# Kernel tuning notes

Hardware: AMD Instinct MI355X
Metric: run time of the kernel (lower is better)

## Reference

```python
import jax, jax.numpy as jnp
import numpy as np

MAX_DISP = 192

def _conv(x, w, b=None, stride=1, pad=0):
    y = jax.lax.conv_general_dilated(x, w, (stride, stride), [(pad, pad), (pad, pad)],
                                     dimension_numbers=('NCHW', 'OIHW', 'NCHW'))
    return y if b is None else y + b[None, :, None, None]

def _inorm(x):  # InstanceNorm2d, affine=False
    m = x.mean((2, 3), keepdims=True)
    v = x.var((2, 3), keepdims=True)
    return (x - m) * jax.lax.rsqrt(v + 1e-5)

def _bnorm(x):  # BatchNorm2d at init (gamma=1, beta=0), batch stats
    m = x.mean((0, 2, 3), keepdims=True)
    v = x.var((0, 2, 3), keepdims=True)
    return (x - m) * jax.lax.rsqrt(v + 1e-5)

def _encoder(x, w1, b1, w2, b2, w3, b3, norm):
    # simplified BasicEncoder: two stride-2 convs -> 1/4 resolution, then 1x1 proj
    x = jax.nn.relu(norm(_conv(x, w1, b1, 2, 3)))
    x = jax.nn.relu(norm(_conv(x, w2, b2, 2, 1)))
    return _conv(x, w3, b3, 1, 0)

def _forward(image1, image2, fnet_w1, fnet_b1, fnet_w2, fnet_b2, fnet_w3, fnet_b3,
             cnet_w1, cnet_b1, cnet_w2, cnet_b2, cnet_w3, cnet_b3,
             bform_a, bform_b, bform_cd_w, bform_cd_b,
             gru_wz, gru_bz, gru_wr, gru_br, gru_wq, gru_bq,
             disp_w1, disp_b1, disp_w2, disp_b2):
    i1 = 2.0 * (image1 / 255.0) - 1.0
    i2 = 2.0 * (image2 / 255.0) - 1.0
    fmap1 = _encoder(i1, fnet_w1, fnet_b1, fnet_w2, fnet_b2, fnet_w3, fnet_b3, _inorm)
    fmap2 = _encoder(i2, fnet_w1, fnet_b1, fnet_w2, fnet_b2, fnet_w3, fnet_b3, _inorm)
    hidden = jnp.tanh(_encoder(i1, cnet_w1, cnet_b1, cnet_w2, cnet_b2, cnet_w3, cnet_b3, _bnorm))
    Wf = fmap1.shape[3]
    for d in range(MAX_DISP // 4):  # 48 sequential width-sweep steps, shrinking overlap
        f1 = fmap1[:, :, :, d:]
        f2 = fmap2[:, :, :, :Wf - d] if d > 0 else fmap2
        # BilinearForm: a(x) + b(y) + cd(x*y), all 1x1 convs
        feat = _conv(f1, bform_a) + _conv(f2, bform_b) + _conv(f1 * f2, bform_cd_w, bform_cd_b)
        h = hidden[:, :, :, d:]
        # gru_input = cat(h, feat); ConvGRU cats hidden again -> [h, h, feat] = 96 ch
        hx = jnp.concatenate([h, h, feat], axis=1)
        z = jax.nn.sigmoid(_conv(hx, gru_wz, gru_bz, 1, 1))
        r = jax.nn.sigmoid(_conv(hx, gru_wr, gru_br, 1, 1))
        q = jnp.tanh(_conv(jnp.concatenate([r * h, h, feat], axis=1), gru_wq, gru_bq, 1, 1))
        h = (1.0 - z) * h + z * q
        hidden = hidden.at[:, :, :, d:].set(h)  # in-place scatter back
    # DisparityHead: conv3x3 -> relu -> conv3x3, negated
    return -_conv(jax.nn.relu(_conv(hidden, disp_w1, disp_b1, 1, 1)), disp_w2, disp_b2, 1, 1)

def setup_inputs():
    key = jax.random.key(0)
    ks = jax.random.split(key, 16)
    B, H, W, D = 1, 384, 640, 32
    def n(k, shape, scale=0.05):
        return (jax.random.normal(k, shape) * scale).astype(jnp.float32)
    z = lambda c: jnp.zeros((c,), jnp.float32)
    return {
        'image1': jax.random.uniform(ks[0], (B, 3, H, W), jnp.float32) * 255.0,
        'image2': jax.random.uniform(ks[1], (B, 3, H, W), jnp.float32) * 255.0,
        'fnet_w1': n(ks[2], (D, 3, 7, 7)), 'fnet_b1': z(D),
        'fnet_w2': n(ks[3], (D, D, 3, 3)), 'fnet_b2': z(D),
        'fnet_w3': n(ks[4], (D, D, 1, 1)), 'fnet_b3': z(D),
        'cnet_w1': n(ks[5], (D, 3, 7, 7)), 'cnet_b1': z(D),
        'cnet_w2': n(ks[6], (D, D, 3, 3)), 'cnet_b2': z(D),
        'cnet_w3': n(ks[7], (D, D, 1, 1)), 'cnet_b3': z(D),
        'bform_a': n(ks[8], (D, D, 1, 1)), 'bform_b': n(ks[9], (D, D, 1, 1)),
        'bform_cd_w': n(ks[10], (D, D, 1, 1)), 'bform_cd_b': z(D),
        'gru_wz': n(ks[11], (D, 3 * D, 3, 3)), 'gru_bz': z(D),
        'gru_wr': n(ks[12], (D, 3 * D, 3, 3)), 'gru_br': z(D),
        'gru_wq': n(ks[13], (D, 3 * D, 3, 3)), 'gru_bq': z(D),
        'disp_w1': n(ks[14], (64, D, 3, 3)), 'disp_b1': z(64),
        'disp_w2': n(ks[15], (1, 64, 3, 3)), 'disp_b2': z(1),
    }

def reference(image1, image2, fnet_w1, fnet_b1, fnet_w2, fnet_b2, fnet_w3, fnet_b3,
              cnet_w1, cnet_b1, cnet_w2, cnet_b2, cnet_w3, cnet_b3,
              bform_a, bform_b, bform_cd_w, bform_cd_b,
              gru_wz, gru_bz, gru_wr, gru_br, gru_wq, gru_bq,
              disp_w1, disp_b1, disp_w2, disp_b2):
    return _forward(image1, image2, fnet_w1, fnet_b1, fnet_w2, fnet_b2, fnet_w3, fnet_b3,
                    cnet_w1, cnet_b1, cnet_w2, cnet_b2, cnet_w3, cnet_b3,
                    bform_a, bform_b, bform_cd_w, bform_cd_b,
                    gru_wz, gru_bz, gru_wr, gru_br, gru_wq, gru_bq,
                    disp_w1, disp_b1, disp_w2, disp_b2)
```

## Files before the change

### kernel.cpp

```cpp
#include <hip/hip_runtime.h>
#include <math.h>

#define H0 384
#define W0 640
#define H1 192
#define W1 320
#define H2 96
#define W2 160
#define NP1 (H1*W1)
#define NP2 (H2*W2)
#define ND  48
#define NBLK2 (NP2/256)
#define CHW ((size_t)32*NP2)
#define PW 162
#define PH 98
#define PSL (PH*PW)
#define PCHW ((size_t)32*PSL)

typedef float v2f __attribute__((ext_vector_type(2)));


__global__ void zero_buf_kernel(float* __restrict__ p, size_t n) {
    size_t i = (size_t)blockIdx.x*256 + threadIdx.x;
    size_t stride = (size_t)gridDim.x*256;
    for (; i < n; i += stride) p[i] = 0.f;
}

__global__ void transpose_w_kernel(const float* __restrict__ in, float* __restrict__ out,
                                   int CI, int K, int CO) {
    int idx = blockIdx.x*256 + threadIdx.x;
    int total = CI*K*CO;
    if (idx >= total) return;
    int co = idx % CO;
    int t  = idx / CO;
    int k  = t % K;
    int ci = t / K;
    out[idx] = in[(co*CI + ci)*K + k];
}

__global__ void prep_zr_pk(const float* __restrict__ wz, const float* __restrict__ wr,
                           float4* __restrict__ wpk) {
    int idx = blockIdx.x*256 + threadIdx.x;
    if (idx >= 16*64*9) return;
    int k  = idx % 9;
    int ci = (idx/9) % 64;
    int cg = idx / (9*64);
    int co0 = cg*2, co1 = co0 + 1;
    float z0, z1, r0, r1;
    if (ci < 32) {
        z0 = wz[(co0*96 + ci)*9 + k] + wz[(co0*96 + ci + 32)*9 + k];
        z1 = wz[(co1*96 + ci)*9 + k] + wz[(co1*96 + ci + 32)*9 + k];
        r0 = wr[(co0*96 + ci)*9 + k] + wr[(co0*96 + ci + 32)*9 + k];
        r1 = wr[(co1*96 + ci)*9 + k] + wr[(co1*96 + ci + 32)*9 + k];
    } else {
        z0 = wz[(co0*96 + ci + 32)*9 + k];
        z1 = wz[(co1*96 + ci + 32)*9 + k];
        r0 = wr[(co0*96 + ci + 32)*9 + k];
        r1 = wr[(co1*96 + ci + 32)*9 + k];
    }
    wpk[idx] = make_float4(z0, z1, r0, r1);
}

__global__ void prep_q_pk(const float* __restrict__ wq, float2* __restrict__ qpk) {
    int idx = blockIdx.x*256 + threadIdx.x;
    if (idx >= 16*96*9) return;
    int k  = idx % 9;
    int ci = (idx/9) % 96;
    int cg = idx / (9*96);
    qpk[idx] = make_float2(wq[((cg*2)*96 + ci)*9 + k], wq[((cg*2+1)*96 + ci)*9 + k]);
}

__global__ void pad_init_kernel(const float* __restrict__ hidden, float* __restrict__ hwork) {
    int idx = blockIdx.x*256 + threadIdx.x;
    if (idx >= 32*PSL) return;
    int c = idx / PSL;
    int r = idx % PSL;
    int py = r / PW, px = r % PW;
    int y = py - 1, x = px - 1;
    float v = 0.f;
    if ((unsigned)y < (unsigned)H2 && (unsigned)x < (unsigned)W2)
        v = hidden[c*NP2 + y*W2 + x];
    hwork[idx] = v;
}


__global__ void conv7s2_v2(const float* __restrict__ img, const float* __restrict__ wt,
                           const float* __restrict__ b, float* __restrict__ out) {
    int sp = blockIdx.x*256 + threadIdx.x;
    int oy = sp / W1, ox = sp % W1;
    float acc[32];
    #pragma unroll
    for (int j = 0; j < 32; ++j) acc[j] = b[j];
    for (int ci = 0; ci < 3; ++ci) {
        for (int ky = 0; ky < 7; ++ky) {
            int iy = 2*oy - 3 + ky;
            if ((unsigned)iy >= (unsigned)H0) continue;
            const float* row  = img + ci*(H0*W0) + iy*W0;
            const float* wrow = wt + (ci*49 + ky*7)*32;
            #pragma unroll
            for (int kx = 0; kx < 7; ++kx) {
                int ix = 2*ox - 3 + kx;
                if ((unsigned)ix >= (unsigned)W0) continue;
                float v = row[ix]*(2.0f/255.0f) - 1.0f;
                const float4* wp = (const float4*)(wrow + kx*32);
                #pragma unroll
                for (int j4 = 0; j4 < 8; ++j4) {
                    float4 w4 = wp[j4];
                    acc[4*j4+0] += v*w4.x; acc[4*j4+1] += v*w4.y;
                    acc[4*j4+2] += v*w4.z; acc[4*j4+3] += v*w4.w;
                }
            }
        }
    }
    #pragma unroll
    for (int j = 0; j < 32; ++j) out[j*NP1 + sp] = acc[j];
}

__global__ void stats_partial_kernel(const float* __restrict__ x, int N, float* __restrict__ st) {
    int c = blockIdx.x >> 3, sl = blockIdx.x & 7;
    int chunk = N >> 3;
    const float4* p = (const float4*)(x + (size_t)c*N + (size_t)sl*chunk);
    int n4 = chunk >> 2;
    float s = 0.f, s2 = 0.f;
    for (int i = threadIdx.x; i < n4; i += 256) {
        float4 v = p[i];
        s  += v.x + v.y + v.z + v.w;
        s2 += v.x*v.x + v.y*v.y + v.z*v.z + v.w*v.w;
    }
    __shared__ float sh1[256], sh2[256];
    sh1[threadIdx.x] = s; sh2[threadIdx.x] = s2;
    __syncthreads();
    for (int o = 128; o > 0; o >>= 1) {
        if (threadIdx.x < o) { sh1[threadIdx.x] += sh1[threadIdx.x+o]; sh2[threadIdx.x] += sh2[threadIdx.x+o]; }
        __syncthreads();
    }
    if (threadIdx.x == 0) { atomicAdd(&st[2*c], sh1[0]); atomicAdd(&st[2*c+1], sh2[0]); }
}

__global__ void norm_relu_v2(float* __restrict__ x, const float* __restrict__ st, int N) {
    int c = blockIdx.y;
    float m    = st[2*c] / (float)N;
    float var  = st[2*c+1] / (float)N - m*m;
    float rstd = rsqrtf(var + 1e-5f);
    float4* p = (float4*)(x + (size_t)c*N);
    int i = blockIdx.x*256 + threadIdx.x;
    float4 v = p[i];
    v.x = fmaxf((v.x-m)*rstd, 0.f); v.y = fmaxf((v.y-m)*rstd, 0.f);
    v.z = fmaxf((v.z-m)*rstd, 0.f); v.w = fmaxf((v.w-m)*rstd, 0.f);
    p[i] = v;
}

__global__ void conv3s2_v2(const float* __restrict__ in, const float* __restrict__ wt,
                           const float* __restrict__ b, float* __restrict__ out) {
    int cg = blockIdx.x / (NP2/256);
    int sp = (blockIdx.x % (NP2/256))*256 + threadIdx.x;
    int co8 = cg*8;
    int oy = sp / W2, ox = sp % W2;
    float acc[8];
    #pragma unroll
    for (int j = 0; j < 8; ++j) acc[j] = b[co8+j];
    for (int ci = 0; ci < 32; ++ci) {
        const float* ip  = in + ci*NP1;
        const float* wci = wt + ci*9*32 + co8;
        #pragma unroll
        for (int ky = 0; ky < 3; ++ky) {
            int iy = 2*oy - 1 + ky;
            if ((unsigned)iy >= (unsigned)H1) continue;
            const float* row = ip + iy*W1;
            #pragma unroll
            for (int kx = 0; kx < 3; ++kx) {
                int ix = 2*ox - 1 + kx;
                if ((unsigned)ix >= (unsigned)W1) continue;
                float v = row[ix];
                const float4* wp = (const float4*)(wci + (ky*3+kx)*32);
                float4 w0 = wp[0], w1 = wp[1];
                acc[0] += v*w0.x; acc[1] += v*w0.y; acc[2] += v*w0.z; acc[3] += v*w0.w;
                acc[4] += v*w1.x; acc[5] += v*w1.y; acc[6] += v*w1.z; acc[7] += v*w1.w;
            }
        }
    }
    #pragma unroll
    for (int j = 0; j < 8; ++j) out[(co8+j)*NP2 + sp] = acc[j];
}

__global__ void conv1x1_v2(const float* __restrict__ in, const float* __restrict__ wt,
                           const float* __restrict__ b, float* __restrict__ out, int mode) {
    int cg = blockIdx.x / (NP2/256);
    int sp = (blockIdx.x % (NP2/256))*256 + threadIdx.x;
    int co8 = cg*8;
    float acc[8];
    #pragma unroll
    for (int j = 0; j < 8; ++j) acc[j] = b[co8+j];
    for (int ci = 0; ci < 32; ++ci) {
        float v = in[ci*NP2 + sp];
        const float4* wp = (const float4*)(wt + ci*32 + co8);
        float4 w0 = wp[0], w1 = wp[1];
        acc[0] += v*w0.x; acc[1] += v*w0.y; acc[2] += v*w0.z; acc[3] += v*w0.w;
        acc[4] += v*w1.x; acc[5] += v*w1.y; acc[6] += v*w1.z; acc[7] += v*w1.w;
    }
    #pragma unroll
    for (int j = 0; j < 8; ++j) {
        float a = acc[j];
        if (mode) a = tanhf(a);
        out[(co8+j)*NP2 + sp] = a;
    }
}


__global__ void feat0_pad_kernel(const float* __restrict__ fmap1, const float* __restrict__ fmap2,
                                 const float* __restrict__ wat, const float* __restrict__ wbt,
                                 const float* __restrict__ wct, const float* __restrict__ bc,
                                 float* __restrict__ featA) {
    int cg  = blockIdx.x / NBLK2;
    int sp  = (blockIdx.x % NBLK2)*256 + threadIdx.x;
    int y = sp / W2;
    int gx = sp % W2;
    int co8 = cg*8;
    float acc[8];
    #pragma unroll
    for (int j = 0; j < 8; ++j) acc[j] = bc[co8+j];
    for (int ci = 0; ci < 32; ++ci) {
        float f1 = fmap1[ci*NP2 + sp];
        float f2 = fmap2[ci*NP2 + sp];
        float f12 = f1*f2;
        const float4* ap = (const float4*)(wat + ci*32 + co8);
        const float4* bp = (const float4*)(wbt + ci*32 + co8);
        const float4* cp = (const float4*)(wct + ci*32 + co8);
        float4 a0 = ap[0], a1 = ap[1];
        float4 b0 = bp[0], b1 = bp[1];
        float4 c0 = cp[0], c1 = cp[1];
        acc[0] += f1*a0.x + f2*b0.x + f12*c0.x;
        acc[1] += f1*a0.y + f2*b0.y + f12*c0.y;
        acc[2] += f1*a0.z + f2*b0.z + f12*c0.z;
        acc[3] += f1*a0.w + f2*b0.w + f12*c0.w;
        acc[4] += f1*a1.x + f2*b1.x + f12*c1.x;
        acc[5] += f1*a1.y + f2*b1.y + f12*c1.y;
        acc[6] += f1*a1.z + f2*b1.z + f12*c1.z;
        acc[7] += f1*a1.w + f2*b1.w + f12*c1.w;
    }
    float* dst = featA + (size_t)(y+1)*PW + (gx+1);
    #pragma unroll
    for (int j = 0; j < 8; ++j) dst[(size_t)(co8+j)*PSL] = acc[j];
}


__global__ __launch_bounds__(256, 4)
void zrf_v5(const float* __restrict__ hworkA, const float* __restrict__ featA,
            const float* __restrict__ fmap1, const float* __restrict__ fmap2,
            const float4* __restrict__ wzrpk,
            const float* __restrict__ wat, const float* __restrict__ wbt,
            const float* __restrict__ wct, const float* __restrict__ bfc,
            const float* __restrict__ bz, const float* __restrict__ br,
            float* __restrict__ zbuf, float* __restrict__ rhpad,
            float* __restrict__ featB, int d) {
    __shared__ v2f lwz[64*9], lwr[64*9];
    __shared__ v2f lfa[32], lfb[32], lfc[32];
    int cg  = blockIdx.x / 30;
    int sp2 = (blockIdx.x % 30)*256 + threadIdx.x;
    int co0 = cg*2;
    {
        const float4* wsrc = wzrpk + (size_t)cg*576;
        for (int i = threadIdx.x; i < 576; i += 256) {
            float4 w = wsrc[i];
            lwz[i] = (v2f){w.x, w.y};
            lwr[i] = (v2f){w.z, w.w};
        }
        if (threadIdx.x < 32) {
            int ci = threadIdx.x;
            lfa[ci] = (v2f){wat[ci*32+co0], wat[ci*32+co0+1]};
            lfb[ci] = (v2f){wbt[ci*32+co0], wbt[ci*32+co0+1]};
            lfc[ci] = (v2f){wct[ci*32+co0], wct[ci*32+co0+1]};
        }
    }
    __syncthreads();
    int y0 = (sp2 / W2)*2;
    int gx = sp2 % W2;
    size_t poff = (size_t)(y0+1)*PW + (gx+1);

    if (gx == d-1) {
        #pragma unroll
        for (int j = 0; j < 2; ++j) {
            rhpad[(size_t)(co0+j)*PSL + poff]      = 0.f;
            rhpad[(size_t)(co0+j)*PSL + poff + PW] = 0.f;
        }
    }

    int dn = d + 1;
    if (dn < ND) {
        if (gx == dn-1) {
            #pragma unroll
            for (int j = 0; j < 2; ++j) {
                featB[(size_t)(co0+j)*PSL + poff]      = 0.f;
                featB[(size_t)(co0+j)*PSL + poff + PW] = 0.f;
            }
        } else if (gx >= dn) {
            v2f f0 = (v2f){bfc[co0], bfc[co0+1]};
            v2f f1 = f0;
            int base1 = y0*W2 + gx;
            #pragma unroll 2
            for (int ci = 0; ci < 32; ++ci) {
                float a1 = fmap1[ci*NP2 + base1];
                float a2 = fmap1[ci*NP2 + base1 + W2];
                float b1 = fmap2[ci*NP2 + base1 - dn];
                float b2 = fmap2[ci*NP2 + base1 + W2 - dn];
                v2f wa = lfa[ci], wb = lfb[ci], wc = lfc[ci];
                f0 += wa*(v2f){a1,a1} + wb*(v2f){b1,b1} + wc*(v2f){a1*b1,a1*b1};
                f1 += wa*(v2f){a2,a2} + wb*(v2f){b2,b2} + wc*(v2f){a2*b2,a2*b2};
            }
            featB[(size_t)co0*PSL + poff]          = f0.x;
            featB[(size_t)(co0+1)*PSL + poff]      = f0.y;
            featB[(size_t)co0*PSL + poff + PW]     = f1.x;
            featB[(size_t)(co0+1)*PSL + poff + PW] = f1.y;
        }
    }

    if (gx < d) return;

    v2f az0 = (v2f){bz[co0], bz[co0+1]}, az1 = az0;
    v2f ar0 = (v2f){br[co0], br[co0+1]}, ar1 = ar0;
    #pragma unroll
    for (int pass = 0; pass < 2; ++pass) {
        const float* p = (pass == 0 ? hworkA : featA) + poff;
        const v2f* wz = lwz + pass*288;
        const v2f* wr = lwr + pass*288;
        #pragma unroll 2
        for (int ci = 0; ci < 32; ++ci) {
            float v[12];
            #pragma unroll
            for (int r = 0; r < 4; ++r) {
                v[r*3+0] = p[(r-1)*PW - 1];
                v[r*3+1] = p[(r-1)*PW    ];
                v[r*3+2] = p[(r-1)*PW + 1];
            }
            #pragma unroll
            for (int k = 0; k < 9; ++k) {
                int ky = k/3, kx = k - 3*ky;
                float t0 = v[ky*3+kx];
                float t1 = v[(ky+1)*3+kx];
                v2f wzk = wz[k], wrk = wr[k];
                az0 += wzk*(v2f){t0,t0}; az1 += wzk*(v2f){t1,t1};
                ar0 += wrk*(v2f){t0,t0}; ar1 += wrk*(v2f){t1,t1};
            }
            p += PSL;
            wz += 9; wr += 9;
        }
    }
    v2f z0, z1, r0, r1;
    z0.x = 1.f/(1.f + __expf(-az0.x)); z0.y = 1.f/(1.f + __expf(-az0.y));
    z1.x = 1.f/(1.f + __expf(-az1.x)); z1.y = 1.f/(1.f + __expf(-az1.y));
    r0.x = 1.f/(1.f + __expf(-ar0.x)); r0.y = 1.f/(1.f + __expf(-ar0.y));
    r1.x = 1.f/(1.f + __expf(-ar1.x)); r1.y = 1.f/(1.f + __expf(-ar1.y));
    int ub = y0*W2 + gx;
    float h00 = hworkA[(size_t)co0*PSL + poff];
    float h01 = hworkA[(size_t)(co0+1)*PSL + poff];
    float h10 = hworkA[(size_t)co0*PSL + poff + PW];
    float h11 = hworkA[(size_t)(co0+1)*PSL + poff + PW];
    zbuf[(size_t)co0*NP2 + ub]          = z0.x;
    zbuf[(size_t)(co0+1)*NP2 + ub]      = z0.y;
    zbuf[(size_t)co0*NP2 + ub + W2]     = z1.x;
    zbuf[(size_t)(co0+1)*NP2 + ub + W2] = z1.y;
    rhpad[(size_t)co0*PSL + poff]          = r0.x*h00;
    rhpad[(size_t)(co0+1)*PSL + poff]      = r0.y*h01;
    rhpad[(size_t)co0*PSL + poff + PW]     = r1.x*h10;
    rhpad[(size_t)(co0+1)*PSL + poff + PW] = r1.y*h11;
}

__global__ __launch_bounds__(256, 4)
void qup_v5(const float* __restrict__ rhpad, const float* __restrict__ hworkA,
            const float* __restrict__ featA, const float* __restrict__ zbuf,
            const float2* __restrict__ qpk, const float* __restrict__ bq,
            float* __restrict__ hidden, float* __restrict__ hworkB, int d) {
    __shared__ v2f lw[96*9];
    int cg  = blockIdx.x / 30;
    int sp2 = (blockIdx.x % 30)*256 + threadIdx.x;
    int co0 = cg*2;
    {
        const float2* wsrc = qpk + (size_t)cg*864;
        for (int i = threadIdx.x; i < 864; i += 256) {
            float2 w = wsrc[i];
            lw[i] = (v2f){w.x, w.y};
        }
    }
    __syncthreads();
    int y0 = (sp2 / W2)*2;
    int gx = sp2 % W2;
    size_t poff = (size_t)(y0+1)*PW + (gx+1);

    if (gx < d) {
        #pragma unroll
        for (int j = 0; j < 2; ++j) {
            size_t p0 = (size_t)(co0+j)*PSL + poff;
            hworkB[p0]      = hworkA[p0];
            hworkB[p0 + PW] = hworkA[p0 + PW];
        }
        return;
    }

    v2f a0 = (v2f){bq[co0], bq[co0+1]};
    v2f a1 = a0;
    const float* bases[3];
    bases[0] = rhpad; bases[1] = hworkA; bases[2] = featA;
    #pragma unroll
    for (int pass = 0; pass < 3; ++pass) {
        const float* p = bases[pass] + poff;
        const v2f* wp = lw + pass*288;
        #pragma unroll 2
        for (int ci = 0; ci < 32; ++ci) {
            float v[12];
            #pragma unroll
            for (int r = 0; r < 4; ++r) {
                v[r*3+0] = p[(r-1)*PW - 1];
                v[r*3+1] = p[(r-1)*PW    ];
                v[r*3+2] = p[(r-1)*PW + 1];
            }
            #pragma unroll
            for (int k = 0; k < 9; ++k) {
                int ky = k/3, kx = k - 3*ky;
                float t0 = v[ky*3+kx];
                float t1 = v[(ky+1)*3+kx];
                v2f wk = wp[k];
                a0 += wk*(v2f){t0,t0};
                a1 += wk*(v2f){t1,t1};
            }
            p += PSL;
            wp += 9;
        }
    }
    float q00 = tanhf(a0.x), q01 = tanhf(a0.y);
    float q10 = tanhf(a1.x), q11 = tanhf(a1.y);
    int ub = y0*W2 + gx;
    #pragma unroll
    for (int j = 0; j < 2; ++j) {
        float qa = (j == 0) ? q00 : q01;
        float qb = (j == 0) ? q10 : q11;
        size_t pidx = (size_t)(co0+j)*PSL + poff;
        size_t uidx = (size_t)(co0+j)*NP2 + ub;
        float z_a = zbuf[uidx];
        float z_b = zbuf[uidx + W2];
        float h_a = hworkA[pidx];
        float h_b = hworkA[pidx + PW];
        float hn_a = (1.f - z_a)*h_a + z_a*qa;
        float hn_b = (1.f - z_b)*h_b + z_b*qb;
        hidden[uidx]      = hn_a;
        hidden[uidx + W2] = hn_b;
        hworkB[pidx]      = (gx == d) ? 0.f : hn_a;
        hworkB[pidx + PW] = (gx == d) ? 0.f : hn_b;
    }
}


__global__ void disp1_v2(const float* __restrict__ hidden, const float* __restrict__ wt,
                         const float* __restrict__ b, float* __restrict__ out) {
    int cg = blockIdx.x / (NP2/256);
    int sp = (blockIdx.x % (NP2/256))*256 + threadIdx.x;
    int co8 = cg*8;
    int y = sp / W2, x = sp % W2;
    float acc[8];
    #pragma unroll
    for (int j = 0; j < 8; ++j) acc[j] = b[co8+j];
    for (int ci = 0; ci < 32; ++ci) {
        const float* ip = hidden + ci*NP2;
        #pragma unroll
        for (int dy = 0; dy < 3; ++dy) {
            int ys = y + dy - 1;
            if ((unsigned)ys >= (unsigned)H2) continue;
            const float* row = ip + ys*W2;
            #pragma unroll
            for (int dx = 0; dx < 3; ++dx) {
                int xs = x + dx - 1;
                if ((unsigned)xs >= (unsigned)W2) continue;
                float v = row[xs];
                const float4* wp = (const float4*)(wt + (ci*9 + dy*3 + dx)*64 + co8);
                float4 w0 = wp[0], w1 = wp[1];
                acc[0] += v*w0.x; acc[1] += v*w0.y; acc[2] += v*w0.z; acc[3] += v*w0.w;
                acc[4] += v*w1.x; acc[5] += v*w1.y; acc[6] += v*w1.z; acc[7] += v*w1.w;
            }
        }
    }
    #pragma unroll
    for (int j = 0; j < 8; ++j) out[(co8+j)*NP2 + sp] = fmaxf(acc[j], 0.f);
}

__global__ void disp2_part_kernel(const float* __restrict__ in, const float* __restrict__ w,
                                  float* __restrict__ part) {
    __shared__ float lw[8*9];
    int g  = blockIdx.x / NBLK2;
    int sp = (blockIdx.x % NBLK2)*256 + threadIdx.x;
    if (threadIdx.x < 72) lw[threadIdx.x] = w[g*72 + threadIdx.x];
    __syncthreads();
    int y = sp / W2, x = sp % W2;
    float acc = 0.f;
    #pragma unroll
    for (int ci = 0; ci < 8; ++ci) {
        const float* ip = in + (g*8 + ci)*NP2;
        #pragma unroll
        for (int dy = 0; dy < 3; ++dy) {
            int ys = y+dy-1; if ((unsigned)ys >= (unsigned)H2) continue;
            const float* row = ip + ys*W2;
            #pragma unroll
            for (int dx = 0; dx < 3; ++dx) {
                int xs = x+dx-1; if ((unsigned)xs >= (unsigned)W2) continue;
                acc += lw[ci*9+dy*3+dx] * row[xs];
            }
        }
    }
    part[g*NP2 + sp] = acc;
}

__global__ void disp2_comb_kernel(const float* __restrict__ part, const float* __restrict__ b,
                                  float* __restrict__ out) {
    int sp = blockIdx.x*256 + threadIdx.x;
    float acc = b[0];
    #pragma unroll
    for (int g = 0; g < 8; ++g) acc += part[g*NP2 + sp];
    out[sp] = -acc;
}


extern "C" void kernel_launch(void* const* d_in, const int* in_sizes, int n_in,
                              void* d_out, int out_size, void* d_ws, size_t ws_size,
                              hipStream_t stream) {
    const float* image1   = (const float*)d_in[0];
    const float* image2   = (const float*)d_in[1];
    const float* fnet_w1  = (const float*)d_in[2];
    const float* fnet_b1  = (const float*)d_in[3];
    const float* fnet_w2  = (const float*)d_in[4];
    const float* fnet_b2  = (const float*)d_in[5];
    const float* fnet_w3  = (const float*)d_in[6];
    const float* fnet_b3  = (const float*)d_in[7];
    const float* cnet_w1  = (const float*)d_in[8];
    const float* cnet_b1  = (const float*)d_in[9];
    const float* cnet_w2  = (const float*)d_in[10];
    const float* cnet_b2  = (const float*)d_in[11];
    const float* cnet_w3  = (const float*)d_in[12];
    const float* cnet_b3  = (const float*)d_in[13];
    const float* bform_a  = (const float*)d_in[14];
    const float* bform_b  = (const float*)d_in[15];
    const float* bform_cd_w = (const float*)d_in[16];
    const float* bform_cd_b = (const float*)d_in[17];
    const float* gru_wz   = (const float*)d_in[18];
    const float* gru_bz   = (const float*)d_in[19];
    const float* gru_wr   = (const float*)d_in[20];
    const float* gru_br   = (const float*)d_in[21];
    const float* gru_wq   = (const float*)d_in[22];
    const float* gru_bq   = (const float*)d_in[23];
    const float* disp_w1  = (const float*)d_in[24];
    const float* disp_b1  = (const float*)d_in[25];
    const float* disp_w2  = (const float*)d_in[26];
    const float* disp_b2  = (const float*)d_in[27];

    float* ws = (float*)d_ws;
    size_t o = 0;
    float* e1     = ws + o; o += (size_t)32*NP1;
    float* e2     = ws + o; o += CHW;
    float* fmap1  = ws + o; o += CHW;
    float* fmap2  = ws + o; o += CHW;
    float* hidden = ws + o; o += CHW;
    float* zbuf   = ws + o; o += CHW;
    float* hwork0 = ws + o; o += PCHW;
    float* hwork1 = ws + o; o += PCHW;
    float* rhpad  = ws + o; o += PCHW;
    float* feat0  = ws + o; o += PCHW;
    float* feat1  = ws + o; o += PCHW;
    float* stats  = ws + o; o += 384;
    float* wzrpk  = ws + o; o += 16*64*9*4;
    float* wqpk   = ws + o; o += 16*96*9*2;
    float* we1f   = ws + o; o += 3*49*32;
    float* we1c   = ws + o; o += 3*49*32;
    float* we2f   = ws + o; o += 32*9*32;
    float* we2c   = ws + o; o += 32*9*32;
    float* w3f    = ws + o; o += 32*32;
    float* w3c    = ws + o; o += 32*32;
    float* wat    = ws + o; o += 32*32;
    float* wbt    = ws + o; o += 32*32;
    float* wct    = ws + o; o += 32*32;
    float* wd1t   = ws + o; o += 32*9*64;
    float* disp1buf  = e1;
    float* disp2part = e2;

    zero_buf_kernel<<<2, 256, 0, stream>>>(stats, 384);
    transpose_w_kernel<<<(3*49*32+255)/256, 256, 0, stream>>>(fnet_w1, we1f, 3, 49, 32);
    transpose_w_kernel<<<(3*49*32+255)/256, 256, 0, stream>>>(cnet_w1, we1c, 3, 49, 32);
    transpose_w_kernel<<<(32*9*32+255)/256, 256, 0, stream>>>(fnet_w2, we2f, 32, 9, 32);
    transpose_w_kernel<<<(32*9*32+255)/256, 256, 0, stream>>>(cnet_w2, we2c, 32, 9, 32);
    transpose_w_kernel<<<4, 256, 0, stream>>>(fnet_w3, w3f, 32, 1, 32);
    transpose_w_kernel<<<4, 256, 0, stream>>>(cnet_w3, w3c, 32, 1, 32);
    transpose_w_kernel<<<4, 256, 0, stream>>>(bform_a, wat, 32, 1, 32);
    transpose_w_kernel<<<4, 256, 0, stream>>>(bform_b, wbt, 32, 1, 32);
    transpose_w_kernel<<<4, 256, 0, stream>>>(bform_cd_w, wct, 32, 1, 32);
    transpose_w_kernel<<<(32*9*64+255)/256, 256, 0, stream>>>(disp_w1, wd1t, 32, 9, 64);
    prep_zr_pk<<<(16*64*9+255)/256, 256, 0, stream>>>(gru_wz, gru_wr, (float4*)wzrpk);
    prep_q_pk<<<(16*96*9+255)/256, 256, 0, stream>>>(gru_wq, (float2*)wqpk);

    auto encoder = [&](const float* img, const float* w1t, const float* b1,
                       const float* w2t, const float* b2,
                       const float* w3t, const float* b3, float* dst, int mode,
                       float* st1, float* st2) {
        conv7s2_v2<<<NP1/256, 256, 0, stream>>>(img, w1t, b1, e1);
        stats_partial_kernel<<<256, 256, 0, stream>>>(e1, NP1, st1);
        norm_relu_v2<<<dim3(NP1/1024, 32), 256, 0, stream>>>(e1, st1, NP1);
        conv3s2_v2<<<4*(NP2/256), 256, 0, stream>>>(e1, w2t, b2, e2);
        stats_partial_kernel<<<256, 256, 0, stream>>>(e2, NP2, st2);
        norm_relu_v2<<<dim3(NP2/1024, 32), 256, 0, stream>>>(e2, st2, NP2);
        conv1x1_v2<<<4*(NP2/256), 256, 0, stream>>>(e2, w3t, b3, dst, mode);
    };
    encoder(image1, we1f, fnet_b1, we2f, fnet_b2, w3f, fnet_b3, fmap1, 0, stats+0,   stats+64);
    encoder(image2, we1f, fnet_b1, we2f, fnet_b2, w3f, fnet_b3, fmap2, 0, stats+128, stats+192);
    encoder(image1, we1c, cnet_b1, we2c, cnet_b2, w3c, cnet_b3, hidden, 1, stats+256, stats+320);

    pad_init_kernel<<<(32*PSL+255)/256, 256, 0, stream>>>(hidden, hwork0);
    zero_buf_kernel<<<1024, 256, 0, stream>>>(hwork1, PCHW);
    zero_buf_kernel<<<1024, 256, 0, stream>>>(rhpad, PCHW);
    zero_buf_kernel<<<1024, 256, 0, stream>>>(feat0, PCHW);
    zero_buf_kernel<<<1024, 256, 0, stream>>>(feat1, PCHW);
    feat0_pad_kernel<<<4*NBLK2, 256, 0, stream>>>(fmap1, fmap2, wat, wbt, wct,
                                                  bform_cd_b, feat0);

    float* hwA = hwork0; float* hwB = hwork1;
    float* ftA = feat0;  float* ftB = feat1;
    for (int d = 0; d < ND; ++d) {
        zrf_v5<<<16*30, 256, 0, stream>>>(hwA, ftA, fmap1, fmap2, (const float4*)wzrpk,
                                          wat, wbt, wct, bform_cd_b, gru_bz, gru_br,
                                          zbuf, rhpad, ftB, d);
        qup_v5<<<16*30, 256, 0, stream>>>(rhpad, hwA, ftA, zbuf, (const float2*)wqpk,
                                          gru_bq, hidden, hwB, d);
        float* t;
        t = hwA; hwA = hwB; hwB = t;
        t = ftA; ftA = ftB; ftB = t;
    }

    disp1_v2<<<8*(NP2/256), 256, 0, stream>>>(hidden, wd1t, disp_b1, disp1buf);
    disp2_part_kernel<<<8*NBLK2, 256, 0, stream>>>(disp1buf, disp_w2, disp2part);
    disp2_comb_kernel<<<NBLK2, 256, 0, stream>>>(disp2part, disp_b2, (float*)d_out);
}
```

Measured before the change: 3.103 ms.

## Shrink GRU sweep grids to active width, fuse prep kernels, retile encoder and disp convs

The 48 GRU sweep steps now launch grids sized to the shrinking active width (W2-d) and index from column d, so blocks no longer idle on columns already finished and qup no longer copies inactive columns. Final hidden state goes into a padded buffer that the new disp1 kernel reads without bounds checks, caching its weights in LDS and computing two rows per thread. The separate weight-prep and zeroing launches are merged into one kernel and one larger zero pass. The first encoder conv is split across two output-channel groups to raise parallelism. The hfinal buffer only receives interior writes on active columns, so correctness depends on its zeroing and on each column's final write landing at the right step.

```diff
diff --git a/kernel.cpp b/kernel.cpp
--- a/kernel.cpp
+++ b/kernel.cpp
@@ -26,11 +26,8 @@
     for (; i < n; i += stride) p[i] = 0.f;
 }
 
-__global__ void transpose_w_kernel(const float* __restrict__ in, float* __restrict__ out,
-                                   int CI, int K, int CO) {
-    int idx = blockIdx.x*256 + threadIdx.x;
-    int total = CI*K*CO;
-    if (idx >= total) return;
+__device__ __forceinline__ void twr_dev(const float* __restrict__ in, float* __restrict__ out,
+                                        int idx, int CI, int K, int CO) {
     int co = idx % CO;
     int t  = idx / CO;
     int k  = t % K;
@@ -38,36 +35,71 @@
     out[idx] = in[(co*CI + ci)*K + k];
 }
 
-__global__ void prep_zr_pk(const float* __restrict__ wz, const float* __restrict__ wr,
-                           float4* __restrict__ wpk) {
-    int idx = blockIdx.x*256 + threadIdx.x;
-    if (idx >= 16*64*9) return;
-    int k  = idx % 9;
-    int ci = (idx/9) % 64;
-    int cg = idx / (9*64);
-    int co0 = cg*2, co1 = co0 + 1;
-    float z0, z1, r0, r1;
-    if (ci < 32) {
-        z0 = wz[(co0*96 + ci)*9 + k] + wz[(co0*96 + ci + 32)*9 + k];
-        z1 = wz[(co1*96 + ci)*9 + k] + wz[(co1*96 + ci + 32)*9 + k];
-        r0 = wr[(co0*96 + ci)*9 + k] + wr[(co0*96 + ci + 32)*9 + k];
-        r1 = wr[(co1*96 + ci)*9 + k] + wr[(co1*96 + ci + 32)*9 + k];
-    } else {
-        z0 = wz[(co0*96 + ci + 32)*9 + k];
-        z1 = wz[(co1*96 + ci + 32)*9 + k];
-        r0 = wr[(co0*96 + ci + 32)*9 + k];
-        r1 = wr[(co1*96 + ci + 32)*9 + k];
-    }
-    wpk[idx] = make_float4(z0, z1, r0, r1);
-}
-
-__global__ void prep_q_pk(const float* __restrict__ wq, float2* __restrict__ qpk) {
-    int idx = blockIdx.x*256 + threadIdx.x;
-    if (idx >= 16*96*9) return;
-    int k  = idx % 9;
-    int ci = (idx/9) % 96;
-    int cg = idx / (9*96);
-    qpk[idx] = make_float2(wq[((cg*2)*96 + ci)*9 + k], wq[((cg*2+1)*96 + ci)*9 + k]);
+__global__ void prep_all(const float* __restrict__ fnet_w1, const float* __restrict__ cnet_w1,
+                         const float* __restrict__ fnet_w2, const float* __restrict__ cnet_w2,
+                         const float* __restrict__ fnet_w3, const float* __restrict__ cnet_w3,
+                         const float* __restrict__ bform_a, const float* __restrict__ bform_b,
+                         const float* __restrict__ bform_cd_w, const float* __restrict__ disp_w1,
+                         const float* __restrict__ gru_wz, const float* __restrict__ gru_wr,
+                         const float* __restrict__ gru_wq,
+                         float* __restrict__ we1f, float* __restrict__ we1c,
+                         float* __restrict__ we2f, float* __restrict__ we2c,
+                         float* __restrict__ w3f, float* __restrict__ w3c,
+                         float* __restrict__ wat, float* __restrict__ wbt,
+                         float* __restrict__ wct, float* __restrict__ wd1t,
+                         float4* __restrict__ wzrpk, float2* __restrict__ wqpk,
+                         float* __restrict__ stats) {
+    int i = blockIdx.x*256 + threadIdx.x;
+    if (i < 4704) { twr_dev(fnet_w1, we1f, i, 3, 49, 32); return; }
+    i -= 4704;
+    if (i < 4704) { twr_dev(cnet_w1, we1c, i, 3, 49, 32); return; }
+    i -= 4704;
+    if (i < 9216) { twr_dev(fnet_w2, we2f, i, 32, 9, 32); return; }
+    i -= 9216;
+    if (i < 9216) { twr_dev(cnet_w2, we2c, i, 32, 9, 32); return; }
+    i -= 9216;
+    if (i < 1024) { twr_dev(fnet_w3, w3f, i, 32, 1, 32); return; }
+    i -= 1024;
+    if (i < 1024) { twr_dev(cnet_w3, w3c, i, 32, 1, 32); return; }
+    i -= 1024;
+    if (i < 1024) { twr_dev(bform_a, wat, i, 32, 1, 32); return; }
+    i -= 1024;
+    if (i < 1024) { twr_dev(bform_b, wbt, i, 32, 1, 32); return; }
+    i -= 1024;
+    if (i < 1024) { twr_dev(bform_cd_w, wct, i, 32, 1, 32); return; }
+    i -= 1024;
+    if (i < 18432) { twr_dev(disp_w1, wd1t, i, 32, 9, 64); return; }
+    i -= 18432;
+    if (i < 9216) {
+        int k  = i % 9;
+        int ci = (i/9) % 64;
+        int cg = i / (9*64);
+        int co0 = cg*2, co1 = co0 + 1;
+        float z0, z1, r0, r1;
+        if (ci < 32) {
+            z0 = gru_wz[(co0*96 + ci)*9 + k] + gru_wz[(co0*96 + ci + 32)*9 + k];
+            z1 = gru_wz[(co1*96 + ci)*9 + k] + gru_wz[(co1*96 + ci + 32)*9 + k];
+            r0 = gru_wr[(co0*96 + ci)*9 + k] + gru_wr[(co0*96 + ci + 32)*9 + k];
+            r1 = gru_wr[(co1*96 + ci)*9 + k] + gru_wr[(co1*96 + ci + 32)*9 + k];
+        } else {
+            z0 = gru_wz[(co0*96 + ci + 32)*9 + k];
+            z1 = gru_wz[(co1*96 + ci + 32)*9 + k];
+            r0 = gru_wr[(co0*96 + ci + 32)*9 + k];
+            r1 = gru_wr[(co1*96 + ci + 32)*9 + k];
+        }
+        wzrpk[i] = make_float4(z0, z1, r0, r1);
+        return;
+    }
+    i -= 9216;
+    if (i < 13824) {
+        int k  = i % 9;
+        int ci = (i/9) % 96;
+        int cg = i / (9*96);
+        wqpk[i] = make_float2(gru_wq[((cg*2)*96 + ci)*9 + k], gru_wq[((cg*2+1)*96 + ci)*9 + k]);
+        return;
+    }
+    i -= 13824;
+    if (i < 384) stats[i] = 0.f;
 }
 
 __global__ void pad_init_kernel(const float* __restrict__ hidden, float* __restrict__ hwork) {
@@ -84,19 +116,21 @@
 }
 
 
-__global__ void conv7s2_v2(const float* __restrict__ img, const float* __restrict__ wt,
+__global__ void conv7s2_v3(const float* __restrict__ img, const float* __restrict__ wt,
                            const float* __restrict__ b, float* __restrict__ out) {
+    int cg = blockIdx.y;
+    int co16 = cg*16;
     int sp = blockIdx.x*256 + threadIdx.x;
     int oy = sp / W1, ox = sp % W1;
-    float acc[32];
-    #pragma unroll
-    for (int j = 0; j < 32; ++j) acc[j] = b[j];
+    float acc[16];
+    #pragma unroll
+    for (int j = 0; j < 16; ++j) acc[j] = b[co16+j];
     for (int ci = 0; ci < 3; ++ci) {
         for (int ky = 0; ky < 7; ++ky) {
             int iy = 2*oy - 3 + ky;
             if ((unsigned)iy >= (unsigned)H0) continue;
             const float* row  = img + ci*(H0*W0) + iy*W0;
-            const float* wrow = wt + (ci*49 + ky*7)*32;
+            const float* wrow = wt + (ci*49 + ky*7)*32 + co16;
             #pragma unroll
             for (int kx = 0; kx < 7; ++kx) {
                 int ix = 2*ox - 3 + kx;
@@ -104,7 +138,7 @@
                 float v = row[ix]*(2.0f/255.0f) - 1.0f;
                 const float4* wp = (const float4*)(wrow + kx*32);
                 #pragma unroll
-                for (int j4 = 0; j4 < 8; ++j4) {
+                for (int j4 = 0; j4 < 4; ++j4) {
                     float4 w4 = wp[j4];
                     acc[4*j4+0] += v*w4.x; acc[4*j4+1] += v*w4.y;
                     acc[4*j4+2] += v*w4.z; acc[4*j4+3] += v*w4.w;
@@ -113,7 +147,7 @@
         }
     }
     #pragma unroll
-    for (int j = 0; j < 32; ++j) out[j*NP1 + sp] = acc[j];
+    for (int j = 0; j < 16; ++j) out[(co16+j)*NP1 + sp] = acc[j];
 }
 
 __global__ void stats_partial_kernel(const float* __restrict__ x, int N, float* __restrict__ st) {
@@ -245,18 +279,17 @@
 
 
 __global__ __launch_bounds__(256, 4)
-void zrf_v5(const float* __restrict__ hworkA, const float* __restrict__ featA,
+void zrf_v6(const float* __restrict__ hworkA, const float* __restrict__ featA,
             const float* __restrict__ fmap1, const float* __restrict__ fmap2,
             const float4* __restrict__ wzrpk,
             const float* __restrict__ wat, const float* __restrict__ wbt,
             const float* __restrict__ wct, const float* __restrict__ bfc,
             const float* __restrict__ bz, const float* __restrict__ br,
             float* __restrict__ zbuf, float* __restrict__ rhpad,
-            float* __restrict__ featB, int d) {
+            float* __restrict__ featB, int d, int Wd) {
     __shared__ v2f lwz[64*9], lwr[64*9];
     __shared__ v2f lfa[32], lfb[32], lfc[32];
-    int cg  = blockIdx.x / 30;
-    int sp2 = (blockIdx.x % 30)*256 + threadIdx.x;
+    int cg  = blockIdx.y;
     int co0 = cg*2;
     {
         const float4* wsrc = wzrpk + (size_t)cg*576;
@@ -273,27 +306,31 @@
         }
     }
     __syncthreads();
-    int y0 = (sp2 / W2)*2;
-    int gx = sp2 % W2;
+    int sp2 = blockIdx.x*256 + threadIdx.x;
+    if (sp2 >= 48*Wd) return;
+    int rp = sp2 / Wd;
+    int lx = sp2 - rp*Wd;
+    int y0 = rp*2;
+    int gx = d + lx;
     size_t poff = (size_t)(y0+1)*PW + (gx+1);
 
-    if (gx == d-1) {
+    if (lx == 0) {
         #pragma unroll
         for (int j = 0; j < 2; ++j) {
-            rhpad[(size_t)(co0+j)*PSL + poff]      = 0.f;
-            rhpad[(size_t)(co0+j)*PSL + poff + PW] = 0.f;
+            rhpad[(size_t)(co0+j)*PSL + poff - 1]      = 0.f;
+            rhpad[(size_t)(co0+j)*PSL + poff + PW - 1] = 0.f;
         }
     }
 
     int dn = d + 1;
     if (dn < ND) {
-        if (gx == dn-1) {
+        if (lx == 0) {
             #pragma unroll
             for (int j = 0; j < 2; ++j) {
                 featB[(size_t)(co0+j)*PSL + poff]      = 0.f;
                 featB[(size_t)(co0+j)*PSL + poff + PW] = 0.f;
             }
-        } else if (gx >= dn) {
+        } else {
             v2f f0 = (v2f){bfc[co0], bfc[co0+1]};
             v2f f1 = f0;
             int base1 = y0*W2 + gx;
@@ -313,8 +350,6 @@
             featB[(size_t)(co0+1)*PSL + poff + PW] = f1.y;
         }
     }
-
-    if (gx < d) return;
 
     v2f az0 = (v2f){bz[co0], bz[co0+1]}, az1 = az0;
     v2f ar0 = (v2f){br[co0], br[co0+1]}, ar1 = ar0;
@@ -366,13 +401,12 @@
 }
 
 __global__ __launch_bounds__(256, 4)
-void qup_v5(const float* __restrict__ rhpad, const float* __restrict__ hworkA,
+void qup_v6(const float* __restrict__ rhpad, const float* __restrict__ hworkA,
             const float* __restrict__ featA, const float* __restrict__ zbuf,
             const float2* __restrict__ qpk, const float* __restrict__ bq,
-            float* __restrict__ hidden, float* __restrict__ hworkB, int d) {
+            float* __restrict__ hfinal, float* __restrict__ hworkB, int d, int Wd) {
     __shared__ v2f lw[96*9];
-    int cg  = blockIdx.x / 30;
-    int sp2 = (blockIdx.x % 30)*256 + threadIdx.x;
+    int cg  = blockIdx.y;
     int co0 = cg*2;
     {
         const float2* wsrc = qpk + (size_t)cg*864;
@@ -382,27 +416,19 @@
         }
     }
     __syncthreads();
-    int y0 = (sp2 / W2)*2;
-    int gx = sp2 % W2;
+    int sp2 = blockIdx.x*256 + threadIdx.x;
+    if (sp2 >= 48*Wd) return;
+    int rp = sp2 / Wd;
+    int lx = sp2 - rp*Wd;
+    int y0 = rp*2;
+    int gx = d + lx;
     size_t poff = (size_t)(y0+1)*PW + (gx+1);
-
-    if (gx < d) {
-        #pragma unroll
-        for (int j = 0; j < 2; ++j) {
-            size_t p0 = (size_t)(co0+j)*PSL + poff;
-            hworkB[p0]      = hworkA[p0];
-            hworkB[p0 + PW] = hworkA[p0 + PW];
-        }
-        return;
-    }
 
     v2f a0 = (v2f){bq[co0], bq[co0+1]};
     v2f a1 = a0;
-    const float* bases[3];
-    bases[0] = rhpad; bases[1] = hworkA; bases[2] = featA;
     #pragma unroll
     for (int pass = 0; pass < 3; ++pass) {
-        const float* p = bases[pass] + poff;
+        const float* p = (pass == 0 ? rhpad : (pass == 1 ? hworkA : featA)) + poff;
         const v2f* wp = lw + pass*288;
         #pragma unroll 2
         for (int ci = 0; ci < 32; ++ci) {
@@ -441,44 +467,57 @@
         float h_b = hworkA[pidx + PW];
         float hn_a = (1.f - z_a)*h_a + z_a*qa;
         float hn_b = (1.f - z_b)*h_b + z_b*qb;
-        hidden[uidx]      = hn_a;
-        hidden[uidx + W2] = hn_b;
-        hworkB[pidx]      = (gx == d) ? 0.f : hn_a;
-        hworkB[pidx + PW] = (gx == d) ? 0.f : hn_b;
-    }
-}
-
-
-__global__ void disp1_v2(const float* __restrict__ hidden, const float* __restrict__ wt,
-                         const float* __restrict__ b, float* __restrict__ out) {
-    int cg = blockIdx.x / (NP2/256);
-    int sp = (blockIdx.x % (NP2/256))*256 + threadIdx.x;
-    int co8 = cg*8;
-    int y = sp / W2, x = sp % W2;
-    float acc[8];
-    #pragma unroll
-    for (int j = 0; j < 8; ++j) acc[j] = b[co8+j];
+        hfinal[pidx]      = hn_a;
+        hfinal[pidx + PW] = hn_b;
+        hworkB[pidx]      = (lx == 0) ? 0.f : hn_a;
+        hworkB[pidx + PW] = (lx == 0) ? 0.f : hn_b;
+    }
+}
+
+
+__global__ __launch_bounds__(256, 4)
+void disp1_v6(const float* __restrict__ hfinal, const float* __restrict__ wt,
+              const float* __restrict__ b, float* __restrict__ out) {
+    __shared__ float4 lw[288];
+    int cg  = blockIdx.y;
+    int co0 = cg*4;
+    for (int i = threadIdx.x; i < 288; i += 256)
+        lw[i] = *(const float4*)&wt[i*64 + co0];
+    __syncthreads();
+    int sp2 = blockIdx.x*256 + threadIdx.x;
+    int y0 = (sp2 / W2)*2;
+    int gx = sp2 % W2;
+    size_t poff = (size_t)(y0+1)*PW + (gx+1);
+    float4 bb = *(const float4*)&b[co0];
+    float acc0[4] = {bb.x, bb.y, bb.z, bb.w};
+    float acc1[4] = {bb.x, bb.y, bb.z, bb.w};
+    const float* p = hfinal + poff;
+    #pragma unroll 2
     for (int ci = 0; ci < 32; ++ci) {
-        const float* ip = hidden + ci*NP2;
+        float v[12];
         #pragma unroll
-        for (int dy = 0; dy < 3; ++dy) {
-            int ys = y + dy - 1;
-            if ((unsigned)ys >= (unsigned)H2) continue;
-            const float* row = ip + ys*W2;
-            #pragma unroll
-            for (int dx = 0; dx < 3; ++dx) {
-                int xs = x + dx - 1;
-                if ((unsigned)xs >= (unsigned)W2) continue;
-                float v = row[xs];
-                const float4* wp = (const float4*)(wt + (ci*9 + dy*3 + dx)*64 + co8);
-                float4 w0 = wp[0], w1 = wp[1];
-                acc[0] += v*w0.x; acc[1] += v*w0.y; acc[2] += v*w0.z; acc[3] += v*w0.w;
-                acc[4] += v*w1.x; acc[5] += v*w1.y; acc[6] += v*w1.z; acc[7] += v*w1.w;
-            }
-        }
-    }
-    #pragma unroll
-    for (int j = 0; j < 8; ++j) out[(co8+j)*NP2 + sp] = fmaxf(acc[j], 0.f);
+        for (int r = 0; r < 4; ++r) {
+            v[r*3+0] = p[(r-1)*PW - 1];
+            v[r*3+1] = p[(r-1)*PW    ];
+            v[r*3+2] = p[(r-1)*PW + 1];
+        }
+        #pragma unroll
+        for (int k = 0; k < 9; ++k) {
+            int ky = k/3, kx = k - 3*ky;
+            float t0 = v[ky*3+kx];
+            float t1 = v[(ky+1)*3+kx];
+            float4 w = lw[ci*9+k];
+            acc0[0] += t0*w.x; acc0[1] += t0*w.y; acc0[2] += t0*w.z; acc0[3] += t0*w.w;
+            acc1[0] += t1*w.x; acc1[1] += t1*w.y; acc1[2] += t1*w.z; acc1[3] += t1*w.w;
+        }
+        p += PSL;
+    }
+    int ub = y0*W2 + gx;
+    #pragma unroll
+    for (int j = 0; j < 4; ++j) {
+        out[(co0+j)*NP2 + ub]      = fmaxf(acc0[j], 0.f);
+        out[(co0+j)*NP2 + ub + W2] = fmaxf(acc1[j], 0.f);
+    }
 }
 
 __global__ void disp2_part_kernel(const float* __restrict__ in, const float* __restrict__ w,
@@ -562,6 +601,7 @@
     float* rhpad  = ws + o; o += PCHW;
     float* feat0  = ws + o; o += PCHW;
     float* feat1  = ws + o; o += PCHW;
+    float* hfinal = ws + o; o += PCHW;
     float* stats  = ws + o; o += 384;
     float* wzrpk  = ws + o; o += 16*64*9*4;
     float* wqpk   = ws + o; o += 16*96*9*2;
@@ -578,25 +618,17 @@
     float* disp1buf  = e1;
     float* disp2part = e2;
 
-    zero_buf_kernel<<<2, 256, 0, stream>>>(stats, 384);
-    transpose_w_kernel<<<(3*49*32+255)/256, 256, 0, stream>>>(fnet_w1, we1f, 3, 49, 32);
-    transpose_w_kernel<<<(3*49*32+255)/256, 256, 0, stream>>>(cnet_w1, we1c, 3, 49, 32);
-    transpose_w_kernel<<<(32*9*32+255)/256, 256, 0, stream>>>(fnet_w2, we2f, 32, 9, 32);
-    transpose_w_kernel<<<(32*9*32+255)/256, 256, 0, stream>>>(cnet_w2, we2c, 32, 9, 32);
-    transpose_w_kernel<<<4, 256, 0, stream>>>(fnet_w3, w3f, 32, 1, 32);
-    transpose_w_kernel<<<4, 256, 0, stream>>>(cnet_w3, w3c, 32, 1, 32);
-    transpose_w_kernel<<<4, 256, 0, stream>>>(bform_a, wat, 32, 1, 32);
-    transpose_w_kernel<<<4, 256, 0, stream>>>(bform_b, wbt, 32, 1, 32);
-    transpose_w_kernel<<<4, 256, 0, stream>>>(bform_cd_w, wct, 32, 1, 32);
-    transpose_w_kernel<<<(32*9*64+255)/256, 256, 0, stream>>>(disp_w1, wd1t, 32, 9, 64);
-    prep_zr_pk<<<(16*64*9+255)/256, 256, 0, stream>>>(gru_wz, gru_wr, (float4*)wzrpk);
-    prep_q_pk<<<(16*96*9+255)/256, 256, 0, stream>>>(gru_wq, (float2*)wqpk);
+    prep_all<<<(74816 + 255)/256, 256, 0, stream>>>(
+        fnet_w1, cnet_w1, fnet_w2, cnet_w2, fnet_w3, cnet_w3,
+        bform_a, bform_b, bform_cd_w, disp_w1, gru_wz, gru_wr, gru_wq,
+        we1f, we1c, we2f, we2c, w3f, w3c, wat, wbt, wct, wd1t,
+        (float4*)wzrpk, (float2*)wqpk, stats);
 
     auto encoder = [&](const float* img, const float* w1t, const float* b1,
                        const float* w2t, const float* b2,
                        const float* w3t, const float* b3, float* dst, int mode,
                        float* st1, float* st2) {
-        conv7s2_v2<<<NP1/256, 256, 0, stream>>>(img, w1t, b1, e1);
+        conv7s2_v3<<<dim3(NP1/256, 2), 256, 0, stream>>>(img, w1t, b1, e1);
         stats_partial_kernel<<<256, 256, 0, stream>>>(e1, NP1, st1);
         norm_relu_v2<<<dim3(NP1/1024, 32), 256, 0, stream>>>(e1, st1, NP1);
         conv3s2_v2<<<4*(NP2/256), 256, 0, stream>>>(e1, w2t, b2, e2);
@@ -608,28 +640,29 @@
     encoder(image2, we1f, fnet_b1, we2f, fnet_b2, w3f, fnet_b3, fmap2, 0, stats+128, stats+192);
     encoder(image1, we1c, cnet_b1, we2c, cnet_b2, w3c, cnet_b3, hidden, 1, stats+256, stats+320);
 
+    zero_buf_kernel<<<2048, 256, 0, stream>>>(hwork1, 5*PCHW);
     pad_init_kernel<<<(32*PSL+255)/256, 256, 0, stream>>>(hidden, hwork0);
-    zero_buf_kernel<<<1024, 256, 0, stream>>>(hwork1, PCHW);
-    zero_buf_kernel<<<1024, 256, 0, stream>>>(rhpad, PCHW);
-    zero_buf_kernel<<<1024, 256, 0, stream>>>(feat0, PCHW);
-    zero_buf_kernel<<<1024, 256, 0, stream>>>(feat1, PCHW);
     feat0_pad_kernel<<<4*NBLK2, 256, 0, stream>>>(fmap1, fmap2, wat, wbt, wct,
                                                   bform_cd_b, feat0);
 
     float* hwA = hwork0; float* hwB = hwork1;
     float* ftA = feat0;  float* ftB = feat1;
     for (int d = 0; d < ND; ++d) {
-        zrf_v5<<<16*30, 256, 0, stream>>>(hwA, ftA, fmap1, fmap2, (const float4*)wzrpk,
-                                          wat, wbt, wct, bform_cd_b, gru_bz, gru_br,
-                                          zbuf, rhpad, ftB, d);
-        qup_v5<<<16*30, 256, 0, stream>>>(rhpad, hwA, ftA, zbuf, (const float2*)wqpk,
-                                          gru_bq, hidden, hwB, d);
+        int Wd = W2 - d;
+        int nblk = (48*Wd + 255)/256;
+        zrf_v6<<<dim3(nblk, 16), 256, 0, stream>>>(hwA, ftA, fmap1, fmap2,
+                                                   (const float4*)wzrpk,
+                                                   wat, wbt, wct, bform_cd_b,
+                                                   gru_bz, gru_br, zbuf, rhpad, ftB, d, Wd);
+        qup_v6<<<dim3(nblk, 16), 256, 0, stream>>>(rhpad, hwA, ftA, zbuf,
+                                                   (const float2*)wqpk, gru_bq,
+                                                   hfinal, hwB, d, Wd);
         float* t;
         t = hwA; hwA = hwB; hwB = t;
         t = ftA; ftA = ftB; ftB = t;
     }
 
-    disp1_v2<<<8*(NP2/256), 256, 0, stream>>>(hidden, wd1t, disp_b1, disp1buf);
+    disp1_v6<<<dim3(30, 16), 256, 0, stream>>>(hfinal, wd1t, disp_b1, disp1buf);
     disp2_part_kernel<<<8*NBLK2, 256, 0, stream>>>(disp1buf, disp_w2, disp2part);
     disp2_comb_kernel<<<NBLK2, 256, 0, stream>>>(disp2part, disp_b2, (float*)d_out);
 }
```

Measured after the change: 3.010 ms. 1.03x faster.
